# Performance work log

Hardware: AMD Instinct MI355X
Metric: run time of the kernel (lower is better)

Reference implementation:

```python
import jax, jax.numpy as jnp
import numpy as np

EPS = 1e-12  # F.normalize eps
WIN_SIZE = 200
WIN_STEP = 30  # eval mode (training uses 10)
N_WIN = 30     # 31 windows from length-1100 axis, last one dropped


def setup_inputs() -> dict:
    key = jax.random.key(0)
    ks = jax.random.split(key, 6)
    dim, K, out_dim = 128, 64, 256
    N, H, W = 8, 16, 900
    s = 1.0 / np.sqrt(dim)
    return {
        "x": jax.random.normal(ks[0], (N, dim, H, W), dtype=jnp.float32),
        "cluster_centers": jax.random.uniform(ks[1], (K, dim), dtype=jnp.float32),
        "conv_w": jax.random.normal(ks[2], (K, dim), dtype=jnp.float32) * s,
        "conv_b": jax.random.normal(ks[3], (K,), dtype=jnp.float32) * s,
        "mlp_w": jax.random.normal(ks[4], (out_dim, K * dim), dtype=jnp.float32) * s,
        "mlp_b": jax.random.normal(ks[5], (out_dim,), dtype=jnp.float32) * s,
    }


def _l2norm(v, axis):
    return v / jnp.clip(jnp.linalg.norm(v, axis=axis, keepdims=True), EPS)


def reference(x, cluster_centers, conv_w, conv_b, mlp_w, mlp_b):
    N, C, H, W = x.shape
    K = conv_w.shape[0]
    # 1x1 conv -> soft assignment, softmax over clusters (dim=1 after view(N,K,HW))
    logits = jnp.einsum('nchw,kc->nkhw', x, conv_w) + conv_b[None, :, None, None]
    a = jax.nn.softmax(logits, axis=1)  # (N,K,H,W)
    # Fused weighted residual sum over H (torch sums dim=-2 of (N,K,C,H,W)):
    # vlad_pre[n,k,c,w] = sum_h a[n,k,h,w]*x[n,c,h,w] - centers[k,c]*sum_h a[n,k,h,w]
    wx = jnp.einsum('nkhw,nchw->nkcw', a, x)               # (N,K,C,W)
    asum = a.sum(axis=2)                                    # (N,K,W)
    res = wx - cluster_centers[None, :, :, None] * asum[:, :, None, :]
    # circular pad along yaw: [800:] ++ all ++ [:100] -> length 1100
    res = jnp.concatenate([res[..., 800:], res, res[..., :100]], axis=-1)
    # sliding-window sum, size 200 step 30, drop last window -> 30 windows
    cs = jnp.cumsum(res, axis=-1)
    cs = jnp.concatenate([jnp.zeros(res.shape[:-1] + (1,), res.dtype), cs], axis=-1)
    starts = jnp.arange(N_WIN) * WIN_STEP
    win = cs[..., starts + WIN_SIZE] - cs[..., starts]      # (N,K,C,30)
    vlad = jnp.transpose(win, (0, 3, 1, 2)).reshape(N * N_WIN, K, C)
    vlad = _l2norm(vlad, axis=2)                            # intra-norm per cluster
    vlad = _l2norm(vlad.reshape(N * N_WIN, K * C), axis=1)  # global norm
    out = vlad @ mlp_w.T + mlp_b
    out = _l2norm(out, axis=1)
    return out.reshape(N, N_WIN, -1)
```

## Files before the change

### kernel.cpp

```cpp
#include <hip/hip_runtime.h>
#include <cstddef>

#define EPSF 1e-12f
#define NCB 90
#define NT 30
#define ODIM 256
#define DDIM 8192

typedef unsigned short u16;
typedef __attribute__((ext_vector_type(8))) short short8;
typedef __attribute__((ext_vector_type(4))) float float4v;

__device__ inline u16 f2bf(float f) {
  union { float f; unsigned u; } v; v.f = f;
  unsigned r = v.u + 0x7FFFu + ((v.u >> 16) & 1u);
  return (u16)(r >> 16);
}
__device__ inline float bf2f(u16 h) {
  union { unsigned u; float f; } v; v.u = ((unsigned)h) << 16;
  return v.f;
}

__global__ __launch_bounds__(256, 3) void k1_assign(
    const float* __restrict__ x,
    const float* __restrict__ conv_w,
    const float* __restrict__ conv_b,
    float* __restrict__ P,
    float* __restrict__ PA)
{
  __shared__ u16 xtf[4160];
  __shared__ u16 xf[5120];
  __shared__ float As[64 * 33];
  __shared__ u16 afr[2048];
  __shared__ float invs[32];
  __shared__ float pasum[256];

  const int bx0 = blockIdx.x;
  const int id = (bx0 & 7) * 90 + (bx0 >> 3);
  const int n = id / NCB, cb = id - n * NCB;
  const int t = threadIdx.x;
  const int lane = t & 63;
  const int w = t >> 6;

  const float* xn = x + (size_t)n * 1843200 + cb * 10;

  const int colt = w & 1;
  const int kt0 = w >> 1;
  const float bk0 = conv_b[kt0 * 16 + (lane & 15)];
  const float bk1 = conv_b[(kt0 + 2) * 16 + (lane & 15)];

  short8 w0h[4], w0l[4], w1h[4], w1l[4];
  {
    int kr0 = kt0 * 16 + (lane & 15);
    int kr1 = kr0 + 32;
    int cbase = (lane >> 4) << 3;
#pragma unroll
    for (int cb32 = 0; cb32 < 4; ++cb32) {
      const float* wp0 = conv_w + (size_t)kr0 * 128 + cb32 * 32 + cbase;
      const float* wp1 = conv_w + (size_t)kr1 * 128 + cb32 * 32 + cbase;
      union { u16 u[8]; short8 v; } hh, ll;
#pragma unroll
      for (int j = 0; j < 8; ++j) {
        float fv = wp0[j];
        u16 h = f2bf(fv);
        hh.u[j] = h;
        ll.u[j] = f2bf(fv - bf2f(h));
      }
      w0h[cb32] = hh.v; w0l[cb32] = ll.v;
#pragma unroll
      for (int j = 0; j < 8; ++j) {
        float fv = wp1[j];
        u16 h = f2bf(fv);
        hh.u[j] = h;
        ll.u[j] = f2bf(fv - bf2f(h));
      }
      w1h[cb32] = hh.v; w1l[cb32] = ll.v;
    }
  }

  float4v pacc[8];
#pragma unroll
  for (int i = 0; i < 8; ++i) pacc[i] = (float4v){0.f, 0.f, 0.f, 0.f};
  float pak = 0.f;

  float2 xr[8];
#pragma unroll
  for (int s = 0; s < 8; ++s) {
    int e2 = t + 256 * s;
    int c = e2 >> 4, p = e2 & 15;
    int cl = 2 * p;
    int h = cl / 10, wi = cl - 10 * h;
    xr[s] = *(const float2*)(xn + (size_t)c * 14400 + h * 900 + wi);
  }

  for (int cc = 0; cc < 5; ++cc) {
    __syncthreads();
#pragma unroll
    for (int s = 0; s < 8; ++s) {
      int e2 = t + 256 * s;
      int c = e2 >> 4, p = e2 & 15;
      int cl = 2 * p;
      u16 h0 = f2bf(xr[s].x), h1 = f2bf(xr[s].y);
      int ip = (c >> 4) * 640 + (p >> 2) * 160 + (c & 15) * 8 + (cl & 7);
      ushort2 pr; pr.x = h0; pr.y = h1;
      *(ushort2*)&xf[ip] = pr;
      int F = (p >> 3) * 4 + (c >> 5);
      int L = (((c >> 3) & 3) << 4) + (cl & 15);
      int i0 = F * 520 + L * 8 + (c & 7);
      xtf[i0] = h0;
      xtf[i0 + 8] = h1;
    }
    if (cc < 4) {
#pragma unroll
      for (int s = 0; s < 8; ++s) {
        int e2 = t + 256 * s;
        int c = e2 >> 4, p = e2 & 15;
        int g = (cc + 1) * 32 + 2 * p;
        int h = g / 10, wi = g - 10 * h;
        xr[s] = *(const float2*)(xn + (size_t)c * 14400 + h * 900 + wi);
      }
    }
    __syncthreads();

    {
      float4v d0 = (float4v){0.f, 0.f, 0.f, 0.f};
      float4v d1 = (float4v){0.f, 0.f, 0.f, 0.f};
#pragma unroll
      for (int cb32 = 0; cb32 < 4; ++cb32) {
        short8 xa = *(short8*)&xtf[(colt * 4 + cb32) * 520 + lane * 8];
        d0 = __builtin_amdgcn_mfma_f32_16x16x32_bf16(xa, w0h[cb32], d0, 0, 0, 0);
        d0 = __builtin_amdgcn_mfma_f32_16x16x32_bf16(xa, w0l[cb32], d0, 0, 0, 0);
        d1 = __builtin_amdgcn_mfma_f32_16x16x32_bf16(xa, w1h[cb32], d1, 0, 0, 0);
        d1 = __builtin_amdgcn_mfma_f32_16x16x32_bf16(xa, w1l[cb32], d1, 0, 0, 0);
      }
      int colb = colt * 16 + ((lane >> 4) << 2);
      int kr0 = kt0 * 16 + (lane & 15);
      int kr1 = kr0 + 32;
#pragma unroll
      for (int r = 0; r < 4; ++r) {
        As[kr0 * 33 + colb + r] = d0[r] + bk0;
        As[kr1 * 33 + colb + r] = d1[r] + bk1;
      }
    }
    __syncthreads();

    {
      const int col8 = lane & 7;
      const int kq = lane >> 3;
      const int colg = w * 8 + col8;
      float m = -3.4e38f;
#pragma unroll
      for (int i = 0; i < 8; ++i) m = fmaxf(m, As[(kq * 8 + i) * 33 + colg]);
      m = fmaxf(m, __shfl_xor(m, 8));
      m = fmaxf(m, __shfl_xor(m, 16));
      m = fmaxf(m, __shfl_xor(m, 32));
      float s = 0.f;
#pragma unroll
      for (int i = 0; i < 8; ++i) {
        int a = (kq * 8 + i) * 33 + colg;
        float e = __expf(As[a] - m);
        As[a] = e;
        s += e;
      }
      s += __shfl_xor(s, 8);
      s += __shfl_xor(s, 16);
      s += __shfl_xor(s, 32);
      if (kq == 0) invs[w * 8 + col8] = 1.f / s;
    }
    {
      union { u16 u[8]; short8 v; } cvt;
      float paks = 0.f;
#pragma unroll
      for (int j = 0; j < 8; ++j) {
        float a = As[lane * 33 + w * 8 + j] * invs[w * 8 + j];
        paks += a;
        cvt.u[j] = f2bf(a);
      }
      pak += paks;
      int dst = ((lane >> 4) * 64 + (w << 4) + (lane & 15)) * 8;
      *(short8*)&afr[dst] = cvt.v;
    }
    __syncthreads();

    {
      short8 aa = *(short8*)&afr[(w * 64 + lane) * 8];
#pragma unroll
      for (int ct = 0; ct < 8; ++ct) {
        short8 xb = *(short8*)&xf[ct * 640 + (lane >> 4) * 160 + (lane & 15) * 8];
        pacc[ct] = __builtin_amdgcn_mfma_f32_16x16x32_bf16(aa, xb, pacc[ct], 0, 0, 0);
      }
    }
  }

  float* Pp = P + (size_t)(n * NCB + cb) * DDIM;
  {
    int krow = w * 16 + ((lane >> 4) << 2);
    int c0 = lane & 15;
#pragma unroll
    for (int ct = 0; ct < 8; ++ct)
#pragma unroll
      for (int r = 0; r < 4; ++r)
        Pp[(krow + r) * 128 + ct * 16 + c0] = pacc[ct][r];
  }
  pasum[t] = pak;
  __syncthreads();
  if (t < 64)
    PA[(size_t)(n * NCB + cb) * 64 + t] =
        pasum[t] + pasum[64 + t] + pasum[128 + t] + pasum[192 + t];
}

__global__ __launch_bounds__(256) void k2_vlad(
    const float* __restrict__ P, const float* __restrict__ PA,
    const float* __restrict__ centers, u16* __restrict__ vlad16,
    float* __restrict__ gss)
{
  __shared__ float Ak[8];
  __shared__ float red[4];
  const int bx0 = blockIdx.x;
  const int id = (bx0 & 7) * 240 + (bx0 >> 3);
  const int n = id / 240;
  const int rem = id - n * 240;
  const int wt = rem >> 3, eb = rem & 7;
  const int win = n * NT + wt;
  const int t = threadIdx.x;

  if (t < 32) {
    int kk = t >> 2, ii = t & 3;
    float s = 0.f;
#pragma unroll
    for (int ss = 0; ss < 5; ++ss) {
      int i = ii + 4 * ss;
      int cb = (3 * wt + 80 + i) % 90;
      s += PA[((size_t)n * NCB + cb) * 64 + eb * 8 + kk];
    }
    s += __shfl_xor(s, 1);
    s += __shfl_xor(s, 2);
    if (ii == 0) Ak[kk] = s;
  }
  __syncthreads();

  const int e0 = eb * 1024 + t * 4;
  const float* base = P + (size_t)n * NCB * DDIM + e0;
  float v[4];
#pragma unroll
  for (int j = 0; j < 4; ++j) v[j] = 0.f;
#pragma unroll 5
  for (int i = 0; i < 20; ++i) {
    int cb = (3 * wt + 80 + i) % 90;
    float4 u0 = *(const float4*)(base + (size_t)cb * DDIM);
    v[0] += u0.x; v[1] += u0.y; v[2] += u0.z; v[3] += u0.w;
  }

  const float A = Ak[t >> 5];
  const float* ce = centers + e0;
  float ss8 = 0.f;
#pragma unroll
  for (int j = 0; j < 4; ++j) {
    float val = v[j] - ce[j] * A;
    v[j] = val;
    ss8 += val * val;
  }
  float ssg = ss8;
  ssg += __shfl_xor(ssg, 1);
  ssg += __shfl_xor(ssg, 2);
  ssg += __shfl_xor(ssg, 4);
  ssg += __shfl_xor(ssg, 8);
  ssg += __shfl_xor(ssg, 16);
  float rn = 1.f / fmaxf(sqrtf(ssg), EPSF);
  float ts = ss8 * rn * rn;
  ts += __shfl_xor(ts, 1);
  ts += __shfl_xor(ts, 2);
  ts += __shfl_xor(ts, 4);
  ts += __shfl_xor(ts, 8);
  ts += __shfl_xor(ts, 16);
  ts += __shfl_xor(ts, 32);
  if ((t & 63) == 0) red[t >> 6] = ts;
  __syncthreads();
  if (t == 0) gss[(size_t)win * 8 + eb] = red[0] + red[1] + red[2] + red[3];

  union { u16 u[4]; ushort4 v4; } o;
#pragma unroll
  for (int j = 0; j < 4; ++j) o.u[j] = f2bf(v[j] * rn);
  *(ushort4*)(vlad16 + (size_t)win * DDIM + e0) = o.v4;
}

__global__ __launch_bounds__(256) void k3_gemm(
    const u16* __restrict__ vlad16, const float* __restrict__ gss,
    const float* __restrict__ mlp_w, float* __restrict__ part)
{
  __shared__ float ga[16];
  const int bx = blockIdx.x;
  const int rt = bx % 15;
  const int h = bx / 15;
  const int ot = h & 1;
  const int ks = h >> 1;
  const int t = threadIdx.x;
  const int lane = t & 63;
  const int w = t >> 6;

  if (t < 16) {
    int r = rt * 16 + t;
    float s = 0.f;
#pragma unroll
    for (int j = 0; j < 8; ++j) s += gss[(size_t)r * 8 + j];
    ga[t] = 1.f / fmaxf(sqrtf(s), EPSF);
  }
  __syncthreads();

  const int m = lane & 15;
  const int kg = lane >> 4;
  const int d0 = ks * 256 + kg * 8;
  const u16* arow = vlad16 + (size_t)(rt * 16 + m) * DDIM + d0;

  float4v acc[2];
#pragma unroll
  for (int i = 0; i < 2; ++i) acc[i] = (float4v){0.f, 0.f, 0.f, 0.f};

#pragma unroll
  for (int ko = 0; ko < 8; ++ko) {
    short8 a = *(const short8*)(arow + ko * 32);
#pragma unroll
    for (int nt = 0; nt < 2; ++nt) {
      int o = ot * 128 + w * 32 + nt * 16 + m;
      const float* wrow = mlp_w + (size_t)o * DDIM + d0 + ko * 32;
      float4 u0 = *(const float4*)wrow;
      float4 u1 = *(const float4*)(wrow + 4);
      union { u16 u[8]; short8 v; } bb;
      bb.u[0] = f2bf(u0.x); bb.u[1] = f2bf(u0.y); bb.u[2] = f2bf(u0.z); bb.u[3] = f2bf(u0.w);
      bb.u[4] = f2bf(u1.x); bb.u[5] = f2bf(u1.y); bb.u[6] = f2bf(u1.z); bb.u[7] = f2bf(u1.w);
      acc[nt] = __builtin_amdgcn_mfma_f32_16x16x32_bf16(a, bb.v, acc[nt], 0, 0, 0);
    }
  }

  float g4[4];
#pragma unroll
  for (int r = 0; r < 4; ++r) g4[r] = ga[kg * 4 + r];
  float* pp = part + ((size_t)ks * 240 + rt * 16) * ODIM;
#pragma unroll
  for (int nt = 0; nt < 2; ++nt) {
    int o = ot * 128 + w * 32 + nt * 16 + m;
#pragma unroll
    for (int r = 0; r < 4; ++r)
      pp[(kg * 4 + r) * ODIM + o] = acc[nt][r] * g4[r];
  }
}

__global__ __launch_bounds__(1024) void k4_out(
    const float* __restrict__ part, const float* __restrict__ bias,
    float* __restrict__ out)
{
  __shared__ float acc[4][256];
  __shared__ float red[4];
  const int r = blockIdx.x;
  const int t = threadIdx.x;
  const int o = t & 255, sq = t >> 8;

  float v = 0.f;
#pragma unroll
  for (int s = 0; s < 8; ++s)
    v += part[((size_t)(sq * 8 + s) * 240 + r) * ODIM + o];
  acc[sq][o] = v;
  __syncthreads();

  float ss = 0.f;
  if (t < 256) {
    v = acc[0][o] + acc[1][o] + acc[2][o] + acc[3][o] + bias[o];
    ss = v * v;
    ss += __shfl_xor(ss, 32);
    ss += __shfl_xor(ss, 16);
    ss += __shfl_xor(ss, 8);
    ss += __shfl_xor(ss, 4);
    ss += __shfl_xor(ss, 2);
    ss += __shfl_xor(ss, 1);
    if ((t & 63) == 0) red[t >> 6] = ss;
  }
  __syncthreads();
  if (t < 256) {
    float total = red[0] + red[1] + red[2] + red[3];
    out[(size_t)r * ODIM + o] = v / fmaxf(sqrtf(total), EPSF);
  }
}

extern "C" void kernel_launch(void* const* d_in, const int* in_sizes, int n_in,
                              void* d_out, int out_size, void* d_ws, size_t ws_size,
                              hipStream_t stream) {
  const float* x       = (const float*)d_in[0];
  const float* centers = (const float*)d_in[1];
  const float* conv_w  = (const float*)d_in[2];
  const float* conv_b  = (const float*)d_in[3];
  const float* mlp_w   = (const float*)d_in[4];
  const float* mlp_b   = (const float*)d_in[5];
  float* out = (float*)d_out;

  float* ws     = (float*)d_ws;
  float* P      = ws;
  float* PA     = ws + 5898240;
  u16*   vlad16 = (u16*)(ws + 5944320);
  float* gss    = (float*)(ws + 6927360);
  float* part   = ws;

  k1_assign<<<dim3(8 * NCB),    dim3(256),  0, stream>>>(x, conv_w, conv_b, P, PA);
  k2_vlad  <<<dim3(8 * NT * 8), dim3(256),  0, stream>>>(P, PA, centers, vlad16, gss);
  k3_gemm  <<<dim3(960),        dim3(256),  0, stream>>>(vlad16, gss, mlp_w, part);
  k4_out   <<<dim3(240),        dim3(1024), 0, stream>>>(part, mlp_b, out);
}
```

Baseline: 172.4 us.

## Process three row tiles per GEMM block to reuse converted weights, with XCD-aware mapping

Each k3_gemm block now handles 48 rows (three 16-row MFMA tiles) instead of 16. Every fp32 mlp_w load and bf16 conversion therefore feeds three MFMAs, and the grid shrinks from 960 to 320 blocks. Block indices are remapped so blocks sharing the same weight slice (h) land on the same XCD, which should improve L2 reuse of mlp_w. The cost is more accumulator registers per thread and fewer blocks to hide latency.

```diff
diff --git a/kernel.cpp b/kernel.cpp
--- a/kernel.cpp
+++ b/kernel.cpp
@@ -288,18 +288,20 @@
     const u16* __restrict__ vlad16, const float* __restrict__ gss,
     const float* __restrict__ mlp_w, float* __restrict__ part)
 {
-  __shared__ float ga[16];
+  __shared__ float ga[48];
   const int bx = blockIdx.x;
-  const int rt = bx % 15;
-  const int h = bx / 15;
+  const int xcd = bx & 7;
+  const int q = bx >> 3;
+  const int rtg = q % 5;
+  const int h = (q / 5) * 8 + xcd;
   const int ot = h & 1;
   const int ks = h >> 1;
   const int t = threadIdx.x;
   const int lane = t & 63;
   const int w = t >> 6;
 
-  if (t < 16) {
-    int r = rt * 16 + t;
+  if (t < 48) {
+    int r = rtg * 48 + t;
     float s = 0.f;
 #pragma unroll
     for (int j = 0; j < 8; ++j) s += gss[(size_t)r * 8 + j];
@@ -310,15 +312,20 @@
   const int m = lane & 15;
   const int kg = lane >> 4;
   const int d0 = ks * 256 + kg * 8;
-  const u16* arow = vlad16 + (size_t)(rt * 16 + m) * DDIM + d0;
-
-  float4v acc[2];
-#pragma unroll
-  for (int i = 0; i < 2; ++i) acc[i] = (float4v){0.f, 0.f, 0.f, 0.f};
+  const u16* a0 = vlad16 + (size_t)(rtg * 48 + m) * DDIM + d0;
+
+  float4v acc[3][2];
+#pragma unroll
+  for (int mi = 0; mi < 3; ++mi)
+#pragma unroll
+    for (int i = 0; i < 2; ++i) acc[mi][i] = (float4v){0.f, 0.f, 0.f, 0.f};
 
 #pragma unroll
   for (int ko = 0; ko < 8; ++ko) {
-    short8 a = *(const short8*)(arow + ko * 32);
+    short8 a[3];
+#pragma unroll
+    for (int mi = 0; mi < 3; ++mi)
+      a[mi] = *(const short8*)(a0 + (size_t)(mi * 16) * DDIM + ko * 32);
 #pragma unroll
     for (int nt = 0; nt < 2; ++nt) {
       int o = ot * 128 + w * 32 + nt * 16 + m;
@@ -328,21 +335,24 @@
       union { u16 u[8]; short8 v; } bb;
       bb.u[0] = f2bf(u0.x); bb.u[1] = f2bf(u0.y); bb.u[2] = f2bf(u0.z); bb.u[3] = f2bf(u0.w);
       bb.u[4] = f2bf(u1.x); bb.u[5] = f2bf(u1.y); bb.u[6] = f2bf(u1.z); bb.u[7] = f2bf(u1.w);
-      acc[nt] = __builtin_amdgcn_mfma_f32_16x16x32_bf16(a, bb.v, acc[nt], 0, 0, 0);
-    }
-  }
-
-  float g4[4];
-#pragma unroll
-  for (int r = 0; r < 4; ++r) g4[r] = ga[kg * 4 + r];
-  float* pp = part + ((size_t)ks * 240 + rt * 16) * ODIM;
-#pragma unroll
-  for (int nt = 0; nt < 2; ++nt) {
-    int o = ot * 128 + w * 32 + nt * 16 + m;
-#pragma unroll
-    for (int r = 0; r < 4; ++r)
-      pp[(kg * 4 + r) * ODIM + o] = acc[nt][r] * g4[r];
-  }
+#pragma unroll
+      for (int mi = 0; mi < 3; ++mi)
+        acc[mi][nt] = __builtin_amdgcn_mfma_f32_16x16x32_bf16(a[mi], bb.v, acc[mi][nt], 0, 0, 0);
+    }
+  }
+
+  float* pp = part + ((size_t)ks * 240 + rtg * 48) * ODIM;
+#pragma unroll
+  for (int mi = 0; mi < 3; ++mi)
+#pragma unroll
+    for (int nt = 0; nt < 2; ++nt) {
+      int o = ot * 128 + w * 32 + nt * 16 + m;
+#pragma unroll
+      for (int r = 0; r < 4; ++r) {
+        int rl = mi * 16 + kg * 4 + r;
+        pp[rl * ODIM + o] = acc[mi][nt][r] * ga[rl];
+      }
+    }
 }
 
 __global__ __launch_bounds__(1024) void k4_out(
@@ -401,6 +411,6 @@
 
   k1_assign<<<dim3(8 * NCB),    dim3(256),  0, stream>>>(x, conv_w, conv_b, P, PA);
   k2_vlad  <<<dim3(8 * NT * 8), dim3(256),  0, stream>>>(P, PA, centers, vlad16, gss);
-  k3_gemm  <<<dim3(960),        dim3(256),  0, stream>>>(vlad16, gss, mlp_w, part);
+  k3_gemm  <<<dim3(320),        dim3(256),  0, stream>>>(vlad16, gss, mlp_w, part);
   k4_out   <<<dim3(240),        dim3(1024), 0, stream>>>(part, mlp_b, out);
 }
```

After: 172.2 us. About the same (-0.1%).
